# Kernel tuning notes

Hardware: AMD Instinct MI355X
Metric: run time of the kernel (lower is better)

## Reference

```python
import jax, jax.numpy as jnp
import numpy as np


def setup_inputs() -> dict:
    key = jax.random.key(0)
    k1, k2 = jax.random.split(key)
    x = jax.random.normal(k1, (32, 512, 2048), dtype=jnp.float32)
    codebook = jax.random.normal(k2, (1024, 512), dtype=jnp.float32)
    return {"x": x, "codebook": codebook}


def reference(x, codebook):
    # x: [N, width, T], codebook: [nb_code, code_dim], width == code_dim
    N, width, T = x.shape
    nb_code = codebook.shape[0]
    # preprocess: [N, width, T] -> [N*T, width]
    xf = jnp.transpose(x, (0, 2, 1)).reshape(-1, width)
    dist = (jnp.sum(xf * xf, axis=-1, keepdims=True)
            - 2.0 * jnp.matmul(xf, codebook.T)
            + jnp.sum(codebook * codebook, axis=-1)[None, :])
    code_idx = jnp.argmin(dist, axis=-1)  # [N*T]
    # dequantize (embedding gather)
    x_d = codebook[code_idx]  # [N*T, width]
    # perplexity over code usage histogram
    counts = jax.ops.segment_sum(jnp.ones(code_idx.shape, dtype=x.dtype),
                                 code_idx, num_segments=nb_code)
    prob = counts / jnp.sum(counts)
    perplexity = jnp.exp(-jnp.sum(prob * jnp.log(prob + 1e-7)))
    # commitment loss against detached quantized vectors
    commit_loss = jnp.mean((xf - jax.lax.stop_gradient(x_d)) ** 2)
    # straight-through estimator
    out = xf + jax.lax.stop_gradient(x_d - xf)
    out = out.reshape(N, T, width).transpose(0, 2, 1)  # [N, width, T]
    return out, code_idx.reshape(N, T), commit_loss, perplexity
```

## Files before the change

kernel.cpp:

```cpp
#include <hip/hip_runtime.h>
#include <cstddef>
#include <cstdint>

#define N_BATCH 32
#define WIDTH   512
#define T_DIM   2048
#define NB_CODE 1024
#define M_ROWS  65536
#define OUT_ELEMS 33554432
#define IDX_OFF  OUT_ELEMS
#define LOSS_OFF (OUT_ELEMS + M_ROWS)
#define PERP_OFF (LOSS_OFF + 1)
#define MARGIN   0.75f

typedef __attribute__((ext_vector_type(8))) short vshort8;
typedef __attribute__((ext_vector_type(4))) float vfloat4;
typedef __attribute__((ext_vector_type(16))) float vfloat16;

typedef __attribute__((address_space(1))) const uint32_t gu32_t;
typedef __attribute__((address_space(3))) uint32_t lu32_t;
static __device__ __forceinline__ void gload16(const void* g, void* l) {
    __builtin_amdgcn_global_load_lds((gu32_t*)g, (lu32_t*)l, 16, 0, 0);
}

static __device__ __forceinline__ unsigned short f2bf(float f) {
    uint32_t u = __float_as_uint(f);
    uint32_t r = (u + 0x7FFFu + ((u >> 16) & 1u)) >> 16;
    return (unsigned short)r;
}
static __device__ __forceinline__ float bf2f(unsigned short s) {
    return __uint_as_float(((uint32_t)s) << 16);
}


__global__ __launch_bounds__(128) void k_prep(const float* __restrict__ cb,
                                              unsigned short* __restrict__ cbh,
                                              float* __restrict__ cnorm,
                                              int* __restrict__ hist) {
    const int c = blockIdx.x, tid = threadIdx.x;
    float4 v = ((const float4*)(cb + (size_t)c * WIDTH))[tid];
    ushort4 h;
    h.x = f2bf(v.x); h.y = f2bf(v.y); h.z = f2bf(v.z); h.w = f2bf(v.w);
    ((ushort4*)(cbh + (size_t)c * WIDTH))[tid] = h;
    float s = v.x * v.x + v.y * v.y + v.z * v.z + v.w * v.w;
#pragma unroll
    for (int off = 32; off >= 1; off >>= 1) s += __shfl_xor(s, off, 64);
    __shared__ float sw[2];
    if ((tid & 63) == 0) sw[tid >> 6] = s;
    __syncthreads();
    if (tid == 0) { cnorm[c] = sw[0] + sw[1]; hist[c] = 0; }
}

__global__ __launch_bounds__(512, 2) void k_argmin(
    const float* __restrict__ x, const unsigned short* __restrict__ cbh,
    const float* __restrict__ cnorm, uint32_t* __restrict__ cand,
    float* __restrict__ sbest, float* __restrict__ xnorm) {
    __shared__ __align__(16) short lds[2][32768];
    __shared__ __align__(16) float cns[NB_CODE];

    const int tid = threadIdx.x;
    const int wv = tid >> 6, l = tid & 63;
    const int l31 = l & 31, hi = l >> 5;
    const int m = l31 & 15;

    int srcoff[8];
#pragma unroll
    for (int j = 0; j < 8; ++j) {
        const int q = wv * 512 + j * 64 + l;
        const int kb = q >> 10, code = (q >> 4) & 63, s = q & 15;
        srcoff[j] = code * 1024 + kb * 256 + ((s ^ (code & 15)) << 4);
    }

#define STAGE(SP, B) do {                                                     \
    const char* cbbase_ = ((const char*)cbh) + (SP) * 65536;                  \
    short* lb_ = &lds[B][0];                                                  \
    _Pragma("unroll")                                                         \
    for (int j = 0; j < 8; ++j)                                               \
        gload16(cbbase_ + srcoff[j], lb_ + (wv * 512 + j * 64) * 8);          \
} while (0)

    STAGE(0, 0);

    { ((float2*)cns)[tid] = ((const float2*)cnorm)[tid]; }

    const int m0w = blockIdx.x * 256 + wv * 32;
    const int n = m0w >> 11;
    const int tcol = (m0w & 2047) + l31;
    vshort8 xh[32];
    float xn = 0.f;
    {
        const float* xb = x + (size_t)n * WIDTH * T_DIM + (size_t)hi * 8 * T_DIM + tcol;
        union U8 { uint32_t u[4]; vshort8 v; };
#pragma unroll
        for (int ks = 0; ks < 32; ++ks) {
            U8 u;
#pragma unroll
            for (int j = 0; j < 4; ++j) {
                const float f0 = xb[(size_t)(ks * 16 + 2 * j) * T_DIM];
                const float f1 = xb[(size_t)(ks * 16 + 2 * j + 1) * T_DIM];
                xn = fmaf(f0, f0, fmaf(f1, f1, xn));
                asm("v_cvt_pk_bf16_f32 %0, %1, %2" : "=v"(u.u[j]) : "v"(f0), "v"(f1));
            }
            xh[ks] = u.v;
        }
    }
    xn += __shfl_xor(xn, 32, 64);
    if (l < 32) xnorm[m0w + l] = xn;

    const int B34 = (m >> 1) << 4;
    const int base_s = l31 * 128 + ((hi ^ (m & 1)) << 3);

    float b1 = 3.4e38f, b2 = 3.4e38f, b3 = 3.4e38f;
    int i1 = 0, i2 = 0, i3 = 0;

#define INS3(S, C) do {                                                       \
        const bool lt1 = (S) < b1, lt2 = (S) < b2, lt3 = (S) < b3;            \
        b3 = lt3 ? (lt2 ? b2 : (S)) : b3;  i3 = lt3 ? (lt2 ? i2 : (C)) : i3; \
        b2 = lt2 ? (lt1 ? b1 : (S)) : b2;  i2 = lt2 ? (lt1 ? i1 : (C)) : i2; \
        b1 = lt1 ? (S) : b1;               i1 = lt1 ? (C) : i1;              \
    } while (0)

    __syncthreads();

    for (int sp = 0; sp < 16; ++sp) {
        if (sp) {
            asm volatile("s_waitcnt vmcnt(0)" ::: "memory");
            __builtin_amdgcn_s_barrier();
        }
        if (sp < 15) {
            if (sp & 1) STAGE(sp + 1, 0); else STAGE(sp + 1, 1);
        }
        const short* buf = lds[sp & 1];
        vfloat16 acc0 = {}, acc1 = {};
        __builtin_amdgcn_s_setprio(1);
#pragma unroll
        for (int ks = 0; ks < 32; ++ks) {
            const int koff = ((ks >> 3) << 13) + (((ks & 7) << 4) ^ B34);
            vshort8 a0 = *(const vshort8*)&buf[base_s + koff];
            acc0 = __builtin_amdgcn_mfma_f32_32x32x16_bf16(a0, xh[ks], acc0, 0, 0, 0);
            vshort8 a1 = *(const vshort8*)&buf[base_s + koff + 4096];
            acc1 = __builtin_amdgcn_mfma_f32_32x32x16_bf16(a1, xh[ks], acc1, 0, 0, 0);
        }
        __builtin_amdgcn_s_setprio(0);
        const int cb0 = sp * 64;
#pragma unroll
        for (int tl = 0; tl < 2; ++tl) {
#pragma unroll
            for (int g = 0; g < 4; ++g) {
                const int cbase = cb0 + tl * 32 + g * 8 + 4 * hi;
                vfloat4 cn = *(const vfloat4*)&cns[cbase];
#pragma unroll
                for (int j = 0; j < 4; ++j) {
                    const float a = tl ? acc1[g * 4 + j] : acc0[g * 4 + j];
                    const float s = fmaf(-2.f, a, cn[j]);
                    INS3(s, cbase + j);
                }
            }
        }
    }

    {
        const float ob1 = __shfl_xor(b1, 32, 64), ob2 = __shfl_xor(b2, 32, 64), ob3 = __shfl_xor(b3, 32, 64);
        const int oi1 = __shfl_xor(i1, 32, 64), oi2 = __shfl_xor(i2, 32, 64), oi3 = __shfl_xor(i3, 32, 64);
        INS3(ob1, oi1); INS3(ob2, oi2); INS3(ob3, oi3);
    }
    if (l < 32) {
        const uint32_t f2 = (b2 - b1 < MARGIN) ? 1u : 0u;
        const uint32_t f3 = (b3 - b1 < MARGIN) ? 1u : 0u;
        cand[m0w + l] = (uint32_t)i1 | ((uint32_t)i2 << 10) | ((uint32_t)i3 << 20) | (f2 << 30) | (f3 << 31);
        sbest[m0w + l] = b1;
    }
}

__global__ __launch_bounds__(256) void k_rescore(
    const float* __restrict__ x, const float* __restrict__ cb,
    const float* __restrict__ cnorm, const uint32_t* __restrict__ cand,
    int* __restrict__ idx_final, float* __restrict__ sbest) {
    __shared__ int list[64];
    __shared__ int cnt;
    const int tid = threadIdx.x;
    const int m0 = blockIdx.x * 64;
    if (tid == 0) cnt = 0;
    __syncthreads();
    if (tid < 64) {
        const uint32_t wv = cand[m0 + tid];
        if (wv >> 30) { const int p = atomicAdd(&cnt, 1); list[p] = tid; }
        else idx_final[m0 + tid] = (int)(wv & 1023u);
    }
    __syncthreads();
    const int nf = cnt;
    const int w = tid >> 6, lid = tid & 63;
    for (int it = w; it < nf; it += 4) {
        const int row = m0 + list[it];
        const uint32_t wv = cand[row];
        const int j1 = (int)(wv & 1023u), j2 = (int)((wv >> 10) & 1023u), j3 = (int)((wv >> 20) & 1023u);
        const bool nd3 = (wv >> 31) & 1u;
        const int n = row >> 11, t = row & 2047;
        const float* xc = x + (size_t)n * WIDTH * T_DIM + t;
        float xv[8];
#pragma unroll
        for (int e = 0; e < 8; ++e)
            xv[e] = xc[(size_t)(lid * 8 + e) * T_DIM];
        float d1 = 0.f, d2 = 0.f, d3 = 0.f;
        {
            const float* c1 = cb + (size_t)j1 * WIDTH + lid * 8;
            const float* c2 = cb + (size_t)j2 * WIDTH + lid * 8;
            const float* c3 = cb + (size_t)j3 * WIDTH + lid * 8;
            float4 a0 = *(const float4*)c1, a1 = *(const float4*)(c1 + 4);
            d1 = fmaf(xv[0], a0.x, fmaf(xv[1], a0.y, fmaf(xv[2], a0.z, fmaf(xv[3], a0.w,
                 fmaf(xv[4], a1.x, fmaf(xv[5], a1.y, fmaf(xv[6], a1.z, xv[7] * a1.w)))))));
            float4 b0 = *(const float4*)c2, b1v = *(const float4*)(c2 + 4);
            d2 = fmaf(xv[0], b0.x, fmaf(xv[1], b0.y, fmaf(xv[2], b0.z, fmaf(xv[3], b0.w,
                 fmaf(xv[4], b1v.x, fmaf(xv[5], b1v.y, fmaf(xv[6], b1v.z, xv[7] * b1v.w)))))));
            if (nd3) {
                float4 g0 = *(const float4*)c3, g1 = *(const float4*)(c3 + 4);
                d3 = fmaf(xv[0], g0.x, fmaf(xv[1], g0.y, fmaf(xv[2], g0.z, fmaf(xv[3], g0.w,
                     fmaf(xv[4], g1.x, fmaf(xv[5], g1.y, fmaf(xv[6], g1.z, xv[7] * g1.w)))))));
            }
        }
#pragma unroll
        for (int off = 32; off >= 1; off >>= 1) {
            d1 += __shfl_xor(d1, off, 64);
            d2 += __shfl_xor(d2, off, 64);
            d3 += __shfl_xor(d3, off, 64);
        }
        if (lid == 0) {
            int win = j1;
            float qw = fmaf(-2.f, d1, cnorm[j1]);
            const float q2 = fmaf(-2.f, d2, cnorm[j2]);
            if (q2 < qw || (q2 == qw && j2 < win)) { win = j2; qw = q2; }
            if (nd3) {
                const float q3 = fmaf(-2.f, d3, cnorm[j3]);
                if (q3 < qw || (q3 == qw && j3 < win)) { win = j3; qw = q3; }
            }
            idx_final[row] = win;
            sbest[row] = qw;
        }
    }
}

__global__ __launch_bounds__(256) void k_scatter(
    const float* __restrict__ cb, const int* __restrict__ idx,
    float* __restrict__ dout, int* __restrict__ hist) {
    __shared__ int sidx[64];
    __shared__ float tile[64][130];
    const int tid = threadIdx.x;
    const int b = blockIdx.x;
    const int n = b >> 5;
    const int t0 = (b & 31) * 64;
    if (tid < 64) {
        const int m2 = n * T_DIM + t0 + tid;
        const int ii = idx[m2];
        sidx[tid] = ii;
        dout[IDX_OFF + m2] = (float)ii;
        atomicAdd(&hist[ii], 1);
    }
    __syncthreads();
    const int w = tid >> 6, l = tid & 63;
    for (int wc = 0; wc < 4; ++wc) {
#pragma unroll
        for (int rr = 0; rr < 16; ++rr) {
            const int row = w * 16 + rr;
            const float2 v = *(const float2*)(cb + (size_t)sidx[row] * WIDTH + wc * 128 + l * 2);
            *(float2*)&tile[row][l * 2] = v;
        }
        __syncthreads();
#pragma unroll 8
        for (int wwi = 0; wwi < 32; ++wwi) {
            const int ww = wc * 128 + w * 32 + wwi;
            dout[((size_t)n * WIDTH + ww) * T_DIM + t0 + l] = tile[l][w * 32 + wwi];
        }
        __syncthreads();
    }
}

__global__ __launch_bounds__(1024) void k_finalize(
    const int* __restrict__ hist, const float* __restrict__ xnorm,
    const float* __restrict__ sbest, float* __restrict__ dout) {
    const int tid = threadIdx.x;
    float e;
    {
        const float p = (float)hist[tid] * (1.0f / (float)M_ROWS);
        e = p * logf(p + 1e-7f);
    }
    float ls = 0.f;
    for (int i = tid; i < M_ROWS; i += 1024) ls += xnorm[i] + sbest[i];
#pragma unroll
    for (int off = 32; off >= 1; off >>= 1) {
        e += __shfl_xor(e, off, 64);
        ls += __shfl_xor(ls, off, 64);
    }
    __shared__ float se[16], sl[16];
    if ((tid & 63) == 0) { se[tid >> 6] = e; sl[tid >> 6] = ls; }
    __syncthreads();
    if (tid == 0) {
        float E = 0.f, L = 0.f;
#pragma unroll
        for (int i = 0; i < 16; ++i) { E += se[i]; L += sl[i]; }
        dout[LOSS_OFF] = L / (float)OUT_ELEMS;
        dout[PERP_OFF] = expf(-E);
    }
}

extern "C" void kernel_launch(void* const* d_in, const int* in_sizes, int n_in,
                              void* d_out, int out_size, void* d_ws, size_t ws_size,
                              hipStream_t stream) {
    const float* x = (const float*)d_in[0];
    const float* cb = (const float*)d_in[1];
    float* dout = (float*)d_out;
    uint8_t* w = (uint8_t*)d_ws;

    unsigned short* cbh = (unsigned short*)w;
    float* cnorm   = (float*)(w + (1u << 20));
    int*   hist    = (int*)(w + (1u << 20) + 4096);
    uint32_t* cand = (uint32_t*)(w + (1u << 20) + 8192);
    int* idx_final = (int*)(w + (1u << 20) + 8192 + 262144);
    float* sbest   = (float*)(w + (1u << 20) + 8192 + 2 * 262144);
    float* xnorm   = (float*)(w + (1u << 20) + 8192 + 3 * 262144);

    k_prep<<<NB_CODE, 128, 0, stream>>>(cb, cbh, cnorm, hist);
    k_argmin<<<M_ROWS / 256, 512, 0, stream>>>(x, cbh, cnorm, cand, sbest, xnorm);
    k_rescore<<<1024, 256, 0, stream>>>(x, cb, cnorm, cand, idx_final, sbest);
    k_scatter<<<1024, 256, 0, stream>>>(cb, idx_final, dout, hist);
    k_finalize<<<1, 1024, 0, stream>>>(hist, xnorm, sbest, dout);
}
```

Measured before the change: 199.2 us.

## Halve argmin block size and split codebook staging along K into half-tiles

The argmin kernel now runs 256-thread blocks over 128 rows instead of 512-thread blocks over 256 rows. The codebook tile in LDS shrinks to half its K depth per stage, so each 64-code chunk is staged in two halves with double buffering, and the swizzle addressing is rebuilt to match. This cuts LDS per block and allows more blocks per CU. In exchange, every block loads the codebook independently, which doubles total codebook traffic, and there are twice as many barrier and wait points.

```diff
diff --git a/kernel.cpp b/kernel.cpp
--- a/kernel.cpp
+++ b/kernel.cpp
@@ -51,39 +51,39 @@
     if (tid == 0) { cnorm[c] = sw[0] + sw[1]; hist[c] = 0; }
 }
 
-__global__ __launch_bounds__(512, 2) void k_argmin(
+__global__ __launch_bounds__(256) void k_argmin(
     const float* __restrict__ x, const unsigned short* __restrict__ cbh,
     const float* __restrict__ cnorm, uint32_t* __restrict__ cand,
     float* __restrict__ sbest, float* __restrict__ xnorm) {
-    __shared__ __align__(16) short lds[2][32768];
+    __shared__ __align__(16) short lds[2][16384];
     __shared__ __align__(16) float cns[NB_CODE];
 
     const int tid = threadIdx.x;
     const int wv = tid >> 6, l = tid & 63;
     const int l31 = l & 31, hi = l >> 5;
-    const int m = l31 & 15;
 
     int srcoff[8];
 #pragma unroll
     for (int j = 0; j < 8; ++j) {
-        const int q = wv * 512 + j * 64 + l;
-        const int kb = q >> 10, code = (q >> 4) & 63, s = q & 15;
-        srcoff[j] = code * 1024 + kb * 256 + ((s ^ (code & 15)) << 4);
+        const int q = j * 256 + tid;
+        const int kq = q >> 10, code = (q >> 4) & 63, sx = q & 15;
+        const int slot = sx ^ (code & 15);
+        srcoff[j] = code * 1024 + kq * 256 + slot * 16;
     }
 
 #define STAGE(SP, B) do {                                                     \
-    const char* cbbase_ = ((const char*)cbh) + (SP) * 65536;                  \
+    const char* cbbase_ = ((const char*)cbh) + ((SP) >> 1) * 65536 + ((SP) & 1) * 512; \
     short* lb_ = &lds[B][0];                                                  \
     _Pragma("unroll")                                                         \
     for (int j = 0; j < 8; ++j)                                               \
-        gload16(cbbase_ + srcoff[j], lb_ + (wv * 512 + j * 64) * 8);          \
+        gload16(cbbase_ + srcoff[j], lb_ + (j * 256 + tid) * 8);              \
 } while (0)
 
     STAGE(0, 0);
 
-    { ((float2*)cns)[tid] = ((const float2*)cnorm)[tid]; }
-
-    const int m0w = blockIdx.x * 256 + wv * 32;
+    { ((float4*)cns)[tid] = ((const float4*)cnorm)[tid]; }
+
+    const int m0w = blockIdx.x * 128 + wv * 32;
     const int n = m0w >> 11;
     const int tcol = (m0w & 2047) + l31;
     vshort8 xh[32];
@@ -107,8 +107,7 @@
     xn += __shfl_xor(xn, 32, 64);
     if (l < 32) xnorm[m0w + l] = xn;
 
-    const int B34 = (m >> 1) << 4;
-    const int base_s = l31 * 128 + ((hi ^ (m & 1)) << 3);
+    const int sxl = l31 & 15;
 
     float b1 = 3.4e38f, b2 = 3.4e38f, b3 = 3.4e38f;
     int i1 = 0, i2 = 0, i3 = 0;
@@ -122,27 +121,32 @@
 
     __syncthreads();
 
-    for (int sp = 0; sp < 16; ++sp) {
-        if (sp) {
-            asm volatile("s_waitcnt vmcnt(0)" ::: "memory");
-            __builtin_amdgcn_s_barrier();
-        }
-        if (sp < 15) {
-            if (sp & 1) STAGE(sp + 1, 0); else STAGE(sp + 1, 1);
-        }
-        const short* buf = lds[sp & 1];
+    for (int cc = 0; cc < 16; ++cc) {
         vfloat16 acc0 = {}, acc1 = {};
-        __builtin_amdgcn_s_setprio(1);
-#pragma unroll
-        for (int ks = 0; ks < 32; ++ks) {
-            const int koff = ((ks >> 3) << 13) + (((ks & 7) << 4) ^ B34);
-            vshort8 a0 = *(const vshort8*)&buf[base_s + koff];
-            acc0 = __builtin_amdgcn_mfma_f32_32x32x16_bf16(a0, xh[ks], acc0, 0, 0, 0);
-            vshort8 a1 = *(const vshort8*)&buf[base_s + koff + 4096];
-            acc1 = __builtin_amdgcn_mfma_f32_32x32x16_bf16(a1, xh[ks], acc1, 0, 0, 0);
-        }
-        __builtin_amdgcn_s_setprio(0);
-        const int cb0 = sp * 64;
+#pragma unroll
+        for (int kh = 0; kh < 2; ++kh) {
+            const int sp = cc * 2 + kh;
+            if (sp) {
+                asm volatile("s_waitcnt vmcnt(0)" ::: "memory");
+                __builtin_amdgcn_s_barrier();
+            }
+            if (sp < 31) {
+                if (sp & 1) STAGE(sp + 1, 0); else STAGE(sp + 1, 1);
+            }
+            const short* buf = lds[sp & 1];
+            __builtin_amdgcn_s_setprio(1);
+#pragma unroll
+            for (int ks = 0; ks < 16; ++ks) {
+                const int addr0 = (ks >> 3) * 8192 + l31 * 128 +
+                                  (((((ks & 7) << 1) | hi) ^ sxl) << 3);
+                vshort8 a0 = *(const vshort8*)&buf[addr0];
+                acc0 = __builtin_amdgcn_mfma_f32_32x32x16_bf16(a0, xh[kh * 16 + ks], acc0, 0, 0, 0);
+                vshort8 a1 = *(const vshort8*)&buf[addr0 + 4096];
+                acc1 = __builtin_amdgcn_mfma_f32_32x32x16_bf16(a1, xh[kh * 16 + ks], acc1, 0, 0, 0);
+            }
+            __builtin_amdgcn_s_setprio(0);
+        }
+        const int cb0 = cc * 64;
 #pragma unroll
         for (int tl = 0; tl < 2; ++tl) {
 #pragma unroll
@@ -319,7 +323,7 @@
     float* xnorm   = (float*)(w + (1u << 20) + 8192 + 3 * 262144);
 
     k_prep<<<NB_CODE, 128, 0, stream>>>(cb, cbh, cnorm, hist);
-    k_argmin<<<M_ROWS / 256, 512, 0, stream>>>(x, cbh, cnorm, cand, sbest, xnorm);
+    k_argmin<<<M_ROWS / 128, 256, 0, stream>>>(x, cbh, cnorm, cand, sbest, xnorm);
     k_rescore<<<1024, 256, 0, stream>>>(x, cb, cnorm, cand, idx_final, sbest);
     k_scatter<<<1024, 256, 0, stream>>>(cb, idx_final, dout, hist);
     k_finalize<<<1, 1024, 0, stream>>>(hist, xnorm, sbest, dout);
```

New measurement: 231.8 us. +16.4%, slower.

## Fuse rescore, scatter and loss partial reduction into one tail kernel

Applied to the files above, without the earlier changes.

Merges the rescore and scatter kernels into a single tail kernel that keeps each block's final indices and loss terms in shared memory, so the intermediate index and score arrays are no longer written to and reread from global memory. Each block also reduces its 64 loss terms and writes one partial, so the single-block finalize sums 1024 partials instead of looping over 65536 rows. This removes a launch and the serial finalize loop. The cost is more shared memory per block and rescore work concentrated ahead of the scatter inside each block.

```diff
diff --git a/kernel.cpp b/kernel.cpp
--- a/kernel.cpp
+++ b/kernel.cpp
@@ -172,20 +172,27 @@
     }
 }
 
-__global__ __launch_bounds__(256) void k_rescore(
+__global__ __launch_bounds__(256) void k_tail(
     const float* __restrict__ x, const float* __restrict__ cb,
     const float* __restrict__ cnorm, const uint32_t* __restrict__ cand,
-    int* __restrict__ idx_final, float* __restrict__ sbest) {
+    const float* __restrict__ sbest, const float* __restrict__ xnorm,
+    float* __restrict__ dout, int* __restrict__ hist,
+    float* __restrict__ lossPart) {
+    __shared__ int sidx[64];
+    __shared__ float sls[64];
     __shared__ int list[64];
     __shared__ int cnt;
+    __shared__ float tile[64][130];
     const int tid = threadIdx.x;
-    const int m0 = blockIdx.x * 64;
+    const int b = blockIdx.x;
+    const int m0 = b * 64;
     if (tid == 0) cnt = 0;
     __syncthreads();
     if (tid < 64) {
         const uint32_t wv = cand[m0 + tid];
+        sidx[tid] = (int)(wv & 1023u);
+        sls[tid] = xnorm[m0 + tid] + sbest[m0 + tid];
         if (wv >> 30) { const int p = atomicAdd(&cnt, 1); list[p] = tid; }
-        else idx_final[m0 + tid] = (int)(wv & 1023u);
     }
     __syncthreads();
     const int nf = cnt;
@@ -233,30 +240,22 @@
                 const float q3 = fmaf(-2.f, d3, cnorm[j3]);
                 if (q3 < qw || (q3 == qw && j3 < win)) { win = j3; qw = q3; }
             }
-            idx_final[row] = win;
-            sbest[row] = qw;
-        }
-    }
-}
-
-__global__ __launch_bounds__(256) void k_scatter(
-    const float* __restrict__ cb, const int* __restrict__ idx,
-    float* __restrict__ dout, int* __restrict__ hist) {
-    __shared__ int sidx[64];
-    __shared__ float tile[64][130];
-    const int tid = threadIdx.x;
-    const int b = blockIdx.x;
+            sidx[list[it]] = win;
+            sls[list[it]] = xnorm[row] + qw;
+        }
+    }
+    __syncthreads();
+    if (tid < 64) {
+        dout[IDX_OFF + m0 + tid] = (float)sidx[tid];
+        atomicAdd(&hist[sidx[tid]], 1);
+        float ls = sls[tid];
+#pragma unroll
+        for (int off = 32; off >= 1; off >>= 1) ls += __shfl_xor(ls, off, 64);
+        if (tid == 0) lossPart[b] = ls;
+    }
     const int n = b >> 5;
     const int t0 = (b & 31) * 64;
-    if (tid < 64) {
-        const int m2 = n * T_DIM + t0 + tid;
-        const int ii = idx[m2];
-        sidx[tid] = ii;
-        dout[IDX_OFF + m2] = (float)ii;
-        atomicAdd(&hist[ii], 1);
-    }
-    __syncthreads();
-    const int w = tid >> 6, l = tid & 63;
+    const int l = tid & 63;
     for (int wc = 0; wc < 4; ++wc) {
 #pragma unroll
         for (int rr = 0; rr < 16; ++rr) {
@@ -274,17 +273,13 @@
     }
 }
 
-__global__ __launch_bounds__(1024) void k_finalize(
-    const int* __restrict__ hist, const float* __restrict__ xnorm,
-    const float* __restrict__ sbest, float* __restrict__ dout) {
+__global__ __launch_bounds__(1024) void k_fin(
+    const int* __restrict__ hist, const float* __restrict__ lossPart,
+    float* __restrict__ dout) {
     const int tid = threadIdx.x;
-    float e;
-    {
-        const float p = (float)hist[tid] * (1.0f / (float)M_ROWS);
-        e = p * logf(p + 1e-7f);
-    }
-    float ls = 0.f;
-    for (int i = tid; i < M_ROWS; i += 1024) ls += xnorm[i] + sbest[i];
+    const float p = (float)hist[tid] * (1.0f / (float)M_ROWS);
+    float e = p * logf(p + 1e-7f);
+    float ls = lossPart[tid];
 #pragma unroll
     for (int off = 32; off >= 1; off >>= 1) {
         e += __shfl_xor(e, off, 64);
@@ -314,13 +309,12 @@
     float* cnorm   = (float*)(w + (1u << 20));
     int*   hist    = (int*)(w + (1u << 20) + 4096);
     uint32_t* cand = (uint32_t*)(w + (1u << 20) + 8192);
-    int* idx_final = (int*)(w + (1u << 20) + 8192 + 262144);
-    float* sbest   = (float*)(w + (1u << 20) + 8192 + 2 * 262144);
-    float* xnorm   = (float*)(w + (1u << 20) + 8192 + 3 * 262144);
+    float* sbest   = (float*)(w + (1u << 20) + 8192 + 262144);
+    float* xnorm   = (float*)(w + (1u << 20) + 8192 + 2 * 262144);
+    float* lossPart= (float*)(w + (1u << 20) + 8192 + 3 * 262144);
 
     k_prep<<<NB_CODE, 128, 0, stream>>>(cb, cbh, cnorm, hist);
     k_argmin<<<M_ROWS / 256, 512, 0, stream>>>(x, cbh, cnorm, cand, sbest, xnorm);
-    k_rescore<<<1024, 256, 0, stream>>>(x, cb, cnorm, cand, idx_final, sbest);
-    k_scatter<<<1024, 256, 0, stream>>>(cb, idx_final, dout, hist);
-    k_finalize<<<1, 1024, 0, stream>>>(hist, xnorm, sbest, dout);
-}
+    k_tail<<<1024, 256, 0, stream>>>(x, cb, cnorm, cand, sbest, xnorm, dout, hist, lossPart);
+    k_fin<<<1, 1024, 0, stream>>>(hist, lossPart, dout);
+}
```

Result: faster. 171.0 us (-14.2%).
